# Optimization experiments

Hardware: AMD Instinct MI355X
Metric: run time of the kernel (lower is better)

Reference implementation:

```python
import jax, jax.numpy as jnp
import numpy as np

# Model hyperparameters (from init_kwargs)
SIG = 10.0      # kernel length scale 'sig'
C = 0.0         # energy integration constant 'c'
STD = 1.0       # data std 'std'
N_ATOMS = 21    # aspirin-like molecule
T_ROWS = 12000  # n_train * n_perms (permutation-expanded training rows)
DESC = N_ATOMS * (N_ATOMS - 1) // 2  # 210
BATCH = 64


def setup_inputs() -> dict:
    key = jax.random.key(0)
    k1, k2, k3 = jax.random.split(key, 3)
    # Geometries: M x N x 3 Cartesian coordinates (spread out so atoms are distinct)
    Rs = jax.random.normal(k1, (BATCH, N_ATOMS, 3), dtype=jnp.float32) * 2.0
    # Permutation-expanded training descriptors (inverse distances -> positive)
    xs_train = jax.random.uniform(k2, (T_ROWS, DESC), dtype=jnp.float32, minval=0.05, maxval=1.0)
    Jx_alphas = jax.random.normal(k3, (T_ROWS, DESC), dtype=jnp.float32)
    return {"Rs": Rs, "xs_train": xs_train, "Jx_alphas": Jx_alphas}


def reference(Rs, xs_train, Jx_alphas):
    sig = SIG
    q = np.sqrt(5.0) / sig
    M, N, _ = Rs.shape
    i, j = np.tril_indices(N, k=-1)

    # Pairwise atomic displacement vectors and distances. Diagonal is padded with 1
    # (instead of inf as in the torch code) -- every diagonal contribution below is
    # multiplied by an exact zero (expand_tril zeroes the diagonal, diffs diag = 0),
    # so the value is irrelevant but this keeps gradients finite.
    diffs = Rs[:, :, None, :] - Rs[:, None, :, :]          # [M, N, N, 3]
    eye = jnp.eye(N, dtype=Rs.dtype)
    dists = jnp.sqrt(jnp.sum(diffs * diffs, axis=-1) + eye)  # [M, N, N]

    # Inverse-distance descriptor (strict lower triangle)
    xs = 1.0 / dists[:, i, j]                              # [M, DESC]

    # Descriptor-space differences vs all (permuted) training points
    x_diffs = (q * xs)[:, None, :] - q * xs_train[None]    # [M, T, DESC]
    x_dists = jnp.sqrt(jnp.sum(x_diffs * x_diffs, axis=-1))  # [M, T]

    # Matern-5/2 kernel pieces
    exp_xs = (5.0 / (3.0 * sig * sig)) * jnp.exp(-x_dists)   # [M, T]
    dot_x_diff_Jx = jnp.einsum('mtd,td->mt', x_diffs, Jx_alphas)  # [M, T]
    exp_xs_1_x_dists = exp_xs * (1.0 + x_dists)              # [M, T]

    # Descriptor-space force pieces
    F1s_x = jnp.einsum('mt,mtd->md', exp_xs * dot_x_diff_Jx, x_diffs)  # [M, DESC]
    F2s_x = exp_xs_1_x_dists @ Jx_alphas                               # [M, DESC]
    Fs_x = (F1s_x - F2s_x) * STD

    # expand_tril: scatter descriptor-space forces into symmetric NxN with zero diag
    full = jnp.zeros((M, N, N), dtype=Rs.dtype)
    full = full.at[:, i, j].set(Fs_x).at[:, j, i].set(Fs_x)

    # Cartesian forces: sum over first atom index (torch's .sum(dim=1))
    Fs = jnp.einsum('mab,mabk->mbk', full / dists ** 3, diffs)  # [M, N, 3]

    # Energies
    Es = jnp.sum(exp_xs_1_x_dists * dot_x_diff_Jx, axis=-1) / q
    Es = C + Es * STD
    return Es, Fs
```

## Files before the change

### kernel.cpp

```cpp
#include <hip/hip_runtime.h>
#include <hip/hip_fp16.h>
#include <math.h>

#define N_ATOMS 21
#define DESC 210
#define APAD 224
#define T_ROWS 12000
#define BATCH 64
#define NBLK 250
#define TROWS_B 48
#define PCW 216

#define QCONST 0.22360679774997896f
#define K0CONST (1.0f/60.0f)

typedef short bf16x8 __attribute__((ext_vector_type(8)));
typedef float f32x4 __attribute__((ext_vector_type(4)));

__device__ __forceinline__ float u2f(unsigned int u) {
    union { unsigned int u; float f; } x; x.u = u; return x.f;
}
__device__ __forceinline__ unsigned short f2bf(float f) {
    union { float f; unsigned int u; } x; x.f = f;
    unsigned int r = x.u + 0x7fffu + ((x.u >> 16) & 1u);
    return (unsigned short)(r >> 16);
}
__device__ __forceinline__ float bf2f(unsigned short h) {
    return u2f((unsigned int)h << 16);
}

#define BS_OFF 0
#define JS_OFF 22272
#define XT_OFF 44544
#define W_OFF  91136
#define NB_OFF 104448
#define BJ_OFF 104640
#define NA_OFF 104832
#define ES_OFF 105088
#define LDS_SZ 106624

__global__ __launch_bounds__(512) void k_fused(const float* __restrict__ Rs,
                                               const float* __restrict__ Btr,
                                               const float* __restrict__ Jx,
                                               unsigned short* __restrict__ Abf,
                                               float* __restrict__ es_p,
                                               float* __restrict__ rs_p,
                                               __half* __restrict__ pC) {
    __shared__ char lds[LDS_SZ];
    const int blk = blockIdx.x;
    const int t0 = blk * TROWS_B;
    const int tid = threadIdx.x;
    const int lane = tid & 63;
    const int w = __builtin_amdgcn_readfirstlane(tid >> 6);
    const int lr = lane & 15;
    const int kb = lane >> 4;
    const int mt = w & 3;
    const int half = w >> 2;

    {
        float* rl = (float*)(lds + JS_OFF);
        for (int i = tid; i < BATCH * 63; i += 512) rl[i] = Rs[i];
    }
    __syncthreads();
    {
        const float* rl = (const float*)(lds + JS_OFF);
        for (int i = tid; i < BATCH * APAD; i += 512) {
            const int m = i / APAD, p = i - m * APAD;
            unsigned short h = 0;
            if (p < DESC) {
                int ia = (int)((1.0f + sqrtf(1.0f + 8.0f * (float)p)) * 0.5f);
                while (ia * (ia - 1) / 2 > p) --ia;
                while ((ia + 1) * ia / 2 <= p) ++ia;
                int ja = p - ia * (ia - 1) / 2;
                const float* Rm = rl + m * 63;
                float dx = Rm[ia * 3 + 0] - Rm[ja * 3 + 0];
                float dy = Rm[ia * 3 + 1] - Rm[ja * 3 + 1];
                float dz = Rm[ia * 3 + 2] - Rm[ja * 3 + 2];
                h = f2bf(QCONST / sqrtf(dx * dx + dy * dy + dz * dz));
            }
            *(unsigned short*)(lds + XT_OFF + m * 448 + p * 2) = h;
        }
    }
    __syncthreads();
    uint4 au[7];
    {
        const char* ap = lds + XT_OFF + (mt * 16 + lr) * 448 + kb * 16;
#pragma unroll
        for (int k8 = 0; k8 < 7; k8++) au[k8] = *(const uint4*)(ap + k8 * 64);
    }
    {
        const int m = tid >> 3, gl = tid & 7;
        float s = 0.f;
#pragma unroll
        for (int it = 0; it < 4; it++) {
            const int c16 = it * 8 + gl;
            if (c16 < 28) {
                uint4 v = *(const uint4*)(lds + XT_OFF + m * 448 + c16 * 16);
                const unsigned int* vv = (const unsigned int*)&v;
#pragma unroll
                for (int q2 = 0; q2 < 4; q2++) {
                    float lo = u2f(vv[q2] << 16), hi = u2f(vv[q2] & 0xFFFF0000u);
                    s = fmaf(lo, lo, s); s = fmaf(hi, hi, s);
                }
            }
        }
#pragma unroll
        for (int msk = 1; msk < 8; msk <<= 1) s += __shfl_xor(s, msk);
        if (gl == 0) *(float*)(lds + NA_OFF + m * 4) = s;
    }
    if (blk == 0) {
        for (int i = tid; i < BATCH * 28; i += 512) {
            uint4 v = *(const uint4*)(lds + XT_OFF + i * 16);
            *(uint4*)((char*)Abf + i * 16) = v;
        }
    }
    __syncthreads();

#pragma unroll
    for (int pass = 0; pass < 2; ++pass) {
        if (pass == 1 && tid >= 256) break;
        const int g = tid >> 3, gl = tid & 7;
        int arr, row;
        if (pass == 0) { arr = (g >= 48) ? 1 : 0; row = arr ? (g - 48) : g; }
        else           { arr = 1; row = 16 + g; }
        const float* sp = (arr ? Jx : Btr) + (size_t)(t0 + row) * DESC;
        char* const rdst = lds + (arr ? JS_OFF : BS_OFF) + row * 464;
        const int xtc = arr ? (96 + row * 2) : (row * 2);
#pragma unroll
        for (int it = 0; it < 15; it++) {
            const int c = it * 8 + gl;
            if (c < 116) {
                float2 v = make_float2(0.f, 0.f);
                if (c < 105) v = *(const float2*)(sp + 2 * c);
                unsigned short hx = f2bf(v.x), hy = f2bf(v.y);
                *(unsigned int*)(rdst + c * 4) = (unsigned)hx | ((unsigned)hy << 16);
                if (c < 112) {
                    const int d = 2 * c;
                    *(unsigned short*)(lds + XT_OFF + d * 208 + xtc) = hx;
                    *(unsigned short*)(lds + XT_OFF + (d + 1) * 208 + xtc) = hy;
                }
            }
        }
    }
    __syncthreads();

    if (tid < 384) {
        const int row = tid >> 3, gl = tid & 7;
        float nb = 0.f, bj = 0.f;
#pragma unroll
        for (int it = 0; it < 15; it++) {
            const int c = it * 8 + gl;
            if (c < 105) {
                unsigned int ub = *(const unsigned int*)(lds + BS_OFF + row * 464 + c * 4);
                unsigned int uj = *(const unsigned int*)(lds + JS_OFF + row * 464 + c * 4);
                float bx = u2f(ub << 16), by = u2f(ub & 0xFFFF0000u);
                float jx2 = u2f(uj << 16), jy2 = u2f(uj & 0xFFFF0000u);
                nb = fmaf(bx, bx, nb); nb = fmaf(by, by, nb);
                bj = fmaf(bx, jx2, bj); bj = fmaf(by, jy2, bj);
            }
        }
#pragma unroll
        for (int msk = 1; msk < 8; msk <<= 1) { nb += __shfl_xor(nb, msk); bj += __shfl_xor(bj, msk); }
        if (gl == 0) {
            *(float*)(lds + NB_OFF + row * 4) = nb;
            *(float*)(lds + BJ_OFF + row * 4) = bj;
        }
    }

    const int nt0 = (half == 0) ? 0 : 1;
    const int nnt = (half == 0) ? 1 : 2;
    f32x4 accP[2] = {{0.f,0.f,0.f,0.f},{0.f,0.f,0.f,0.f}};
    f32x4 accQ[2] = {{0.f,0.f,0.f,0.f},{0.f,0.f,0.f,0.f}};
#pragma unroll
    for (int k8 = 0; k8 < 7; k8++) {
        union { uint4 u; bf16x8 h; } a;
        a.u = au[k8];
#pragma unroll
        for (int s = 0; s < 2; s++) {
            if (s < nnt) {
                const int nt = nt0 + s;
                union { uint4 u; bf16x8 h; } bu, ju;
                const int ro = (nt * 16 + lr) * 464 + k8 * 64 + kb * 16;
                bu.u = *(const uint4*)(lds + BS_OFF + ro);
                ju.u = *(const uint4*)(lds + JS_OFF + ro);
                accP[s] = __builtin_amdgcn_mfma_f32_16x16x32_bf16(a.h, bu.h, accP[s], 0, 0, 0);
                accQ[s] = __builtin_amdgcn_mfma_f32_16x16x32_bf16(a.h, ju.h, accQ[s], 0, 0, 0);
            }
        }
    }
    __syncthreads();

    float na4[4];
#pragma unroll
    for (int r = 0; r < 4; r++)
        na4[r] = *(const float*)(lds + NA_OFF + (mt * 16 + kb * 4 + r) * 4);
#pragma unroll
    for (int s = 0; s < 2; s++) {
        if (s < nnt) {
            const int nt = nt0 + s;
            const int row = nt * 16 + lr;
            const float nb_c = *(const float*)(lds + NB_OFF + row * 4);
            const float bj_c = *(const float*)(lds + BJ_OFF + row * 4);
            float es4[4], rs4[4];
#pragma unroll
            for (int r = 0; r < 4; r++) {
                float S = na4[r] + QCONST * QCONST * nb_c - 2.f * QCONST * accP[s][r];
                float xd = sqrtf(fmaxf(S, 0.f));
                float e = K0CONST * __expf(-xd);
                float dot = accQ[s][r] - QCONST * bj_c;
                float w1 = e * dot;
                float w2 = e * (1.f + xd);
                es4[r] = w2 * dot; rs4[r] = w1;
                const int mrow = mt * 16 + kb * 4 + r;
                *(unsigned short*)(lds + W_OFF + mrow * 208 + row * 2) = f2bf(QCONST * w1);
                *(unsigned short*)(lds + W_OFF + mrow * 208 + 96 + row * 2) = f2bf(w2);
            }
#pragma unroll
            for (int msk = 1; msk < 16; msk <<= 1) {
#pragma unroll
                for (int r = 0; r < 4; r++) {
                    es4[r] += __shfl_xor(es4[r], msk);
                    rs4[r] += __shfl_xor(rs4[r], msk);
                }
            }
            if (lr == 0) {
#pragma unroll
                for (int r = 0; r < 4; r++) {
                    const int m = mt * 16 + kb * 4 + r;
                    *(float*)(lds + ES_OFF + (nt * 64 + m) * 4) = es4[r];
                    *(float*)(lds + ES_OFF + 768 + (nt * 64 + m) * 4) = rs4[r];
                }
            }
        }
    }
    __syncthreads();

    if (tid < 64) {
        const float* esl = (const float*)(lds + ES_OFF);
        const float* rsl = (const float*)(lds + ES_OFF + 768);
        es_p[(size_t)tid * NBLK + blk] = esl[tid] + esl[64 + tid] + esl[128 + tid];
        rs_p[(size_t)tid * NBLK + blk] = rsl[tid] + rsl[64 + tid] + rsl[128 + tid];
    }

    {
        union { uint4 u; bf16x8 h; } wa[3];
        const char* Wp = lds + W_OFF + (mt * 16 + lr) * 208;
#pragma unroll
        for (int c = 0; c < 3; c++) wa[c].u = *(const uint4*)(Wp + c * 64 + kb * 16);
        __half* D = (__half*)lds;
#pragma unroll
        for (int j = 0; j < 7; j++) {
            const int dt = half * 7 + j;
            const char* Xp = lds + XT_OFF + (dt * 16 + lr) * 208;
            f32x4 acc = {0.f, 0.f, 0.f, 0.f};
#pragma unroll
            for (int c = 0; c < 3; c++) {
                union { uint4 u; bf16x8 h; } xb;
                xb.u = *(const uint4*)(Xp + c * 64 + kb * 16);
                acc = __builtin_amdgcn_mfma_f32_16x16x32_bf16(wa[c].h, xb.h, acc, 0, 0, 0);
            }
#pragma unroll
            for (int r = 0; r < 4; r++)
                D[(mt * 16 + kb * 4 + r) * 224 + dt * 16 + lr] = __float2half(acc[r]);
        }
    }
    __syncthreads();

    {
        const char* D = (const char*)lds;
        for (int i = tid; i < 64 * 27; i += 512) {
            const int mrow = i / 27, oct = i % 27;
            uint4 v = *(const uint4*)(D + mrow * 448 + oct * 16);
            *(uint4*)((char*)pC + (((size_t)mrow * NBLK + blk) * PCW + oct * 8) * 2) = v;
        }
    }
}

__global__ __launch_bounds__(512) void k_final(const float* __restrict__ Rs,
                                               const unsigned short* __restrict__ Abf,
                                               const float* __restrict__ es_p,
                                               const float* __restrict__ rs_p,
                                               const __half* __restrict__ pC,
                                               float* __restrict__ out) {
    const int m = blockIdx.x;
    const int tid = threadIdx.x;
    __shared__ float parts[27][16][8];
    __shared__ float fsx[DESC];
    __shared__ float R[N_ATOMS * 3];
    __shared__ float s_rs, s_es;
    if (tid < N_ATOMS * 3) R[tid] = Rs[m * N_ATOMS * 3 + tid];
    if (tid < 432) {
        const int cg = tid / 27, o = tid % 27;
        float facc[8];
#pragma unroll
        for (int e = 0; e < 8; e++) facc[e] = 0.f;
        const __half* base = pC + (size_t)m * NBLK * PCW + o * 8;
        for (int c = cg; c < NBLK; c += 16) {
            uint4 v = *(const uint4*)(base + (size_t)c * PCW);
            const __half2* h = (const __half2*)&v;
#pragma unroll
            for (int p2 = 0; p2 < 4; p2++) {
                float2 f = __half22float2(h[p2]);
                facc[p2 * 2] += f.x;
                facc[p2 * 2 + 1] += f.y;
            }
        }
#pragma unroll
        for (int e = 0; e < 8; e++) parts[o][cg][e] = facc[e];
    } else if (tid >= 448) {
        const int lx = tid - 448;
        float es = 0.f, rs = 0.f;
        for (int c2 = lx; c2 < NBLK; c2 += 64) {
            es += es_p[(size_t)m * NBLK + c2];
            rs += rs_p[(size_t)m * NBLK + c2];
        }
        for (int msk = 1; msk < 64; msk <<= 1) {
            es += __shfl_xor(es, msk);
            rs += __shfl_xor(rs, msk);
        }
        if (lx == 0) { s_es = es; s_rs = rs; }
    }
    __syncthreads();
    if (tid < DESC) {
        float s = 0.f;
        const int o = tid >> 3, e = tid & 7;
#pragma unroll
        for (int cg = 0; cg < 16; cg++) s += parts[o][cg][e];
        fsx[tid] = s_rs * bf2f(Abf[m * APAD + tid]) - s;
    }
    if (tid == 0) out[m] = s_es * (1.0f / QCONST);
    __syncthreads();
    if (tid < N_ATOMS * 3) {
        const int b = tid / 3, kk = tid % 3;
        float acc = 0.f;
        for (int a = 0; a < N_ATOMS; a++) {
            if (a == b) continue;
            float dx = R[a * 3 + 0] - R[b * 3 + 0];
            float dy = R[a * 3 + 1] - R[b * 3 + 1];
            float dz = R[a * 3 + 2] - R[b * 3 + 2];
            float d2 = dx * dx + dy * dy + dz * dz;
            float dist = sqrtf(d2);
            float inv3 = 1.0f / (d2 * dist);
            int hi = (a > b) ? a : b, lo = (a > b) ? b : a;
            int p = hi * (hi - 1) / 2 + lo;
            float diffk = (kk == 0) ? dx : ((kk == 1) ? dy : dz);
            acc = fmaf(fsx[p] * inv3, diffk, acc);
        }
        out[BATCH + m * N_ATOMS * 3 + tid] = acc;
    }
}

extern "C" void kernel_launch(void* const* d_in, const int* in_sizes, int n_in,
                              void* d_out, int out_size, void* d_ws, size_t ws_size,
                              hipStream_t stream) {
    (void)in_sizes; (void)n_in; (void)out_size; (void)ws_size;
    const float* Rs = (const float*)d_in[0];
    const float* Btr = (const float*)d_in[1];
    const float* Jx = (const float*)d_in[2];
    float* out = (float*)d_out;

    char* ws = (char*)d_ws;
    unsigned short* Abf = (unsigned short*)ws;  ws += (size_t)BATCH * APAD * 2;
    float* es_p = (float*)ws;                   ws += (size_t)BATCH * NBLK * 4;
    float* rs_p = (float*)ws;                   ws += (size_t)BATCH * NBLK * 4;
    __half* pC = (__half*)ws;

    k_fused<<<dim3(NBLK), dim3(512), 0, stream>>>(Rs, Btr, Jx, Abf, es_p, rs_p, pC);
    k_final<<<dim3(BATCH), dim3(512), 0, stream>>>(Rs, Abf, es_p, rs_p, pC, out);
}
```

Measured before the change: 39.90 us.

## Move descriptor computation into a separate prep kernel and batch global loads

Each of the 250 fused blocks previously recomputed the bf16 inverse-distance descriptors and their squared norms for all 64 geometries. A new small prep kernel now computes them once and writes them to the workspace, and the fused kernel reads its A fragments and norms from global memory. The training-row staging loop is also restructured to issue all 14 float2 global loads before converting and storing to LDS, which raises memory-level parallelism. The trade-off is an extra kernel launch and a dependency between the prep and fused kernels.

```diff
diff --git a/kernel.cpp b/kernel.cpp
--- a/kernel.cpp
+++ b/kernel.cpp
@@ -27,6 +27,40 @@
 }
 __device__ __forceinline__ float bf2f(unsigned short h) {
     return u2f((unsigned int)h << 16);
+}
+
+__global__ __launch_bounds__(256) void k_prep(const float* __restrict__ Rs,
+                                              unsigned short* __restrict__ Abf,
+                                              float* __restrict__ na2) {
+    int m = blockIdx.x;
+    __shared__ float R[N_ATOMS * 3];
+    __shared__ float red[256];
+    int tid = threadIdx.x;
+    if (tid < N_ATOMS * 3) R[tid] = Rs[m * N_ATOMS * 3 + tid];
+    __syncthreads();
+    float val = 0.f;
+    if (tid < DESC) {
+        int p = tid;
+        int i = (int)((1.0f + sqrtf(1.0f + 8.0f * (float)p)) * 0.5f);
+        while (i * (i - 1) / 2 > p) --i;
+        while ((i + 1) * i / 2 <= p) ++i;
+        int j = p - i * (i - 1) / 2;
+        float dx = R[i * 3 + 0] - R[j * 3 + 0];
+        float dy = R[i * 3 + 1] - R[j * 3 + 1];
+        float dz = R[i * 3 + 2] - R[j * 3 + 2];
+        float d = sqrtf(dx * dx + dy * dy + dz * dz);
+        val = QCONST / d;
+    }
+    unsigned short h = f2bf(val);
+    if (tid < APAD) Abf[m * APAD + tid] = h;
+    float va = bf2f(h);
+    red[tid] = va * va;
+    __syncthreads();
+    for (int s = 128; s > 0; s >>= 1) {
+        if (tid < s) red[tid] += red[tid + s];
+        __syncthreads();
+    }
+    if (tid == 0) na2[m] = red[0];
 }
 
 #define BS_OFF 0
@@ -39,10 +73,10 @@
 #define ES_OFF 105088
 #define LDS_SZ 106624
 
-__global__ __launch_bounds__(512) void k_fused(const float* __restrict__ Rs,
-                                               const float* __restrict__ Btr,
+__global__ __launch_bounds__(512) void k_fused(const float* __restrict__ Btr,
                                                const float* __restrict__ Jx,
-                                               unsigned short* __restrict__ Abf,
+                                               const unsigned short* __restrict__ Abf,
+                                               const float* __restrict__ na2,
                                                float* __restrict__ es_p,
                                                float* __restrict__ rs_p,
                                                __half* __restrict__ pC) {
@@ -57,64 +91,13 @@
     const int mt = w & 3;
     const int half = w >> 2;
 
-    {
-        float* rl = (float*)(lds + JS_OFF);
-        for (int i = tid; i < BATCH * 63; i += 512) rl[i] = Rs[i];
-    }
-    __syncthreads();
-    {
-        const float* rl = (const float*)(lds + JS_OFF);
-        for (int i = tid; i < BATCH * APAD; i += 512) {
-            const int m = i / APAD, p = i - m * APAD;
-            unsigned short h = 0;
-            if (p < DESC) {
-                int ia = (int)((1.0f + sqrtf(1.0f + 8.0f * (float)p)) * 0.5f);
-                while (ia * (ia - 1) / 2 > p) --ia;
-                while ((ia + 1) * ia / 2 <= p) ++ia;
-                int ja = p - ia * (ia - 1) / 2;
-                const float* Rm = rl + m * 63;
-                float dx = Rm[ia * 3 + 0] - Rm[ja * 3 + 0];
-                float dy = Rm[ia * 3 + 1] - Rm[ja * 3 + 1];
-                float dz = Rm[ia * 3 + 2] - Rm[ja * 3 + 2];
-                h = f2bf(QCONST / sqrtf(dx * dx + dy * dy + dz * dz));
-            }
-            *(unsigned short*)(lds + XT_OFF + m * 448 + p * 2) = h;
-        }
-    }
-    __syncthreads();
     uint4 au[7];
     {
-        const char* ap = lds + XT_OFF + (mt * 16 + lr) * 448 + kb * 16;
-#pragma unroll
-        for (int k8 = 0; k8 < 7; k8++) au[k8] = *(const uint4*)(ap + k8 * 64);
-    }
-    {
-        const int m = tid >> 3, gl = tid & 7;
-        float s = 0.f;
-#pragma unroll
-        for (int it = 0; it < 4; it++) {
-            const int c16 = it * 8 + gl;
-            if (c16 < 28) {
-                uint4 v = *(const uint4*)(lds + XT_OFF + m * 448 + c16 * 16);
-                const unsigned int* vv = (const unsigned int*)&v;
-#pragma unroll
-                for (int q2 = 0; q2 < 4; q2++) {
-                    float lo = u2f(vv[q2] << 16), hi = u2f(vv[q2] & 0xFFFF0000u);
-                    s = fmaf(lo, lo, s); s = fmaf(hi, hi, s);
-                }
-            }
-        }
-#pragma unroll
-        for (int msk = 1; msk < 8; msk <<= 1) s += __shfl_xor(s, msk);
-        if (gl == 0) *(float*)(lds + NA_OFF + m * 4) = s;
-    }
-    if (blk == 0) {
-        for (int i = tid; i < BATCH * 28; i += 512) {
-            uint4 v = *(const uint4*)(lds + XT_OFF + i * 16);
-            *(uint4*)((char*)Abf + i * 16) = v;
-        }
-    }
-    __syncthreads();
+        const unsigned short* ap = Abf + (mt * 16 + lr) * APAD + kb * 8;
+#pragma unroll
+        for (int k8 = 0; k8 < 7; k8++) au[k8] = *(const uint4*)(ap + k8 * 32);
+    }
+    if (tid < 64) *(float*)(lds + NA_OFF + tid * 4) = na2[tid];
 
 #pragma unroll
     for (int pass = 0; pass < 2; ++pass) {
@@ -124,23 +107,28 @@
         if (pass == 0) { arr = (g >= 48) ? 1 : 0; row = arr ? (g - 48) : g; }
         else           { arr = 1; row = 16 + g; }
         const float* sp = (arr ? Jx : Btr) + (size_t)(t0 + row) * DESC;
+        float2 v[14];
+#pragma unroll
+        for (int it = 0; it < 14; ++it) {
+            int c = it * 8 + gl; if (c > 104) c = 104;
+            v[it] = *(const float2*)(sp + 2 * c);
+        }
         char* const rdst = lds + (arr ? JS_OFF : BS_OFF) + row * 464;
-        const int xtc = arr ? (96 + row * 2) : (row * 2);
-#pragma unroll
-        for (int it = 0; it < 15; it++) {
+        const int xtc = (arr ? 96 : 0) + row * 2;
+#pragma unroll
+        for (int it = 0; it < 14; ++it) {
             const int c = it * 8 + gl;
-            if (c < 116) {
-                float2 v = make_float2(0.f, 0.f);
-                if (c < 105) v = *(const float2*)(sp + 2 * c);
-                unsigned short hx = f2bf(v.x), hy = f2bf(v.y);
-                *(unsigned int*)(rdst + c * 4) = (unsigned)hx | ((unsigned)hy << 16);
-                if (c < 112) {
-                    const int d = 2 * c;
-                    *(unsigned short*)(lds + XT_OFF + d * 208 + xtc) = hx;
-                    *(unsigned short*)(lds + XT_OFF + (d + 1) * 208 + xtc) = hy;
-                }
-            }
-        }
+            const bool real = (c < 105);
+            const float2 vv = real ? v[it] : make_float2(0.f, 0.f);
+            const unsigned short hx = f2bf(vv.x), hy = f2bf(vv.y);
+            *(unsigned int*)(rdst + c * 4) = (unsigned)hx | ((unsigned)hy << 16);
+            if (c < 112) {
+                const int d = 2 * c;
+                *(unsigned short*)(lds + XT_OFF + d * 208 + xtc) = hx;
+                *(unsigned short*)(lds + XT_OFF + (d + 1) * 208 + xtc) = hy;
+            }
+        }
+        if (gl < 4) *(unsigned int*)(rdst + (112 + gl) * 4) = 0u;
     }
     __syncthreads();
 
@@ -148,13 +136,13 @@
         const int row = tid >> 3, gl = tid & 7;
         float nb = 0.f, bj = 0.f;
 #pragma unroll
-        for (int it = 0; it < 15; it++) {
+        for (int it = 0; it < 14; ++it) {
             const int c = it * 8 + gl;
             if (c < 105) {
-                unsigned int ub = *(const unsigned int*)(lds + BS_OFF + row * 464 + c * 4);
-                unsigned int uj = *(const unsigned int*)(lds + JS_OFF + row * 464 + c * 4);
-                float bx = u2f(ub << 16), by = u2f(ub & 0xFFFF0000u);
-                float jx2 = u2f(uj << 16), jy2 = u2f(uj & 0xFFFF0000u);
+                const unsigned int ub = *(const unsigned int*)(lds + BS_OFF + row * 464 + c * 4);
+                const unsigned int uj = *(const unsigned int*)(lds + JS_OFF + row * 464 + c * 4);
+                const float bx = u2f(ub << 16), by = u2f(ub & 0xFFFF0000u);
+                const float jx2 = u2f(uj << 16), jy2 = u2f(uj & 0xFFFF0000u);
                 nb = fmaf(bx, bx, nb); nb = fmaf(by, by, nb);
                 bj = fmaf(bx, jx2, bj); bj = fmaf(by, jy2, bj);
             }
@@ -361,10 +349,12 @@
 
     char* ws = (char*)d_ws;
     unsigned short* Abf = (unsigned short*)ws;  ws += (size_t)BATCH * APAD * 2;
+    float* na2 = (float*)ws;                    ws += BATCH * 4;
     float* es_p = (float*)ws;                   ws += (size_t)BATCH * NBLK * 4;
     float* rs_p = (float*)ws;                   ws += (size_t)BATCH * NBLK * 4;
     __half* pC = (__half*)ws;
 
-    k_fused<<<dim3(NBLK), dim3(512), 0, stream>>>(Rs, Btr, Jx, Abf, es_p, rs_p, pC);
+    k_prep<<<dim3(BATCH), dim3(256), 0, stream>>>(Rs, Abf, na2);
+    k_fused<<<dim3(NBLK), dim3(512), 0, stream>>>(Btr, Jx, Abf, na2, es_p, rs_p, pC);
     k_final<<<dim3(BATCH), dim3(512), 0, stream>>>(Rs, Abf, es_p, rs_p, pC, out);
 }
```

Result: faster. 32.43 us (-18.7%).
